# Performance work log

Measured on AMD Instinct MI355X. Metric: run time of the kernel, lower is better.

## Reference

```python
import jax, jax.numpy as jnp
import numpy as np

B, N, M = 2, 2048, 1024
C, CTX, H = 1024, 1024, 16
D = C // H
HID = int(C * 4.0)
EPS = 1e-6


def _ln(h):
    # LayerNorm32: fp32 layernorm, eps=1e-6, no affine params
    h32 = h.astype(jnp.float32)
    mu = jnp.mean(h32, axis=-1, keepdims=True)
    var = jnp.var(h32, axis=-1, keepdims=True)
    return ((h32 - mu) * jax.lax.rsqrt(var + EPS)).astype(h.dtype)


def _sdpa(q, k, v):
    # q: [B,Q,H,D], k/v: [B,K,H,D]
    scale = 1.0 / np.sqrt(D)
    s = jnp.einsum('bqhd,bkhd->bhqk', q, k) * scale
    p = jax.nn.softmax(s, axis=-1)
    return jnp.einsum('bhqk,bkhd->bqhd', p, v)


def _forward(x, context, Wqkv, bqkv, Wos, bos, Wq, bq, Wkv, bkv, Woc, boc, W1, b1, W2, b2):
    Bx, Nx, _ = x.shape
    Mx = context.shape[1]
    # --- self-attention (attn_mode='full') ---
    h = _ln(x)
    qkv = (h @ Wqkv + bqkv).reshape(Bx, Nx, 3, H, D)
    q, k, v = qkv[:, :, 0], qkv[:, :, 1], qkv[:, :, 2]
    a = _sdpa(q, k, v).reshape(Bx, Nx, C)
    x = x + (a @ Wos + bos)
    # --- cross-attention (always 'full') ---
    h = _ln(x)
    q = (h @ Wq + bq).reshape(Bx, Nx, H, D)
    kv = (context @ Wkv + bkv).reshape(Bx, Mx, 2, H, D)
    k, v = kv[:, :, 0], kv[:, :, 1]
    a = _sdpa(q, k, v).reshape(Bx, Nx, C)
    x = x + (a @ Woc + boc)
    # --- FFN with tanh-approx GELU ---
    h = _ln(x)
    x = x + (jax.nn.gelu(h @ W1 + b1, approximate=True) @ W2 + b2)
    return x


def setup_inputs() -> dict:
    key = jax.random.key(0)
    ks = jax.random.split(key, 12)
    rn = lambda k, shape: (jax.random.normal(k, shape, jnp.float32) * 0.02)
    return {
        'x': jax.random.normal(ks[0], (B, N, C), jnp.float32),
        'context': jax.random.normal(ks[1], (B, M, CTX), jnp.float32),
        'Wqkv': rn(ks[2], (C, 3 * C)), 'bqkv': jnp.zeros((3 * C,), jnp.float32),
        'Wos': rn(ks[3], (C, C)), 'bos': jnp.zeros((C,), jnp.float32),
        'Wq': rn(ks[4], (C, C)), 'bq': jnp.zeros((C,), jnp.float32),
        'Wkv': rn(ks[5], (CTX, 2 * C)), 'bkv': jnp.zeros((2 * C,), jnp.float32),
        'Woc': rn(ks[6], (C, C)), 'boc': jnp.zeros((C,), jnp.float32),
        'W1': rn(ks[7], (C, HID)), 'b1': jnp.zeros((HID,), jnp.float32),
        'W2': rn(ks[8], (HID, C)), 'b2': jnp.zeros((C,), jnp.float32),
    }


def reference(x, context, Wqkv, bqkv, Wos, bos, Wq, bq, Wkv, bkv, Woc, boc, W1, b1, W2, b2):
    return _forward(x, context, Wqkv, bqkv, Wos, bos, Wq, bq, Wkv, bkv, Woc, boc, W1, b1, W2, b2)
```

## Files before the change

### kernel.cpp

```cpp
#include <hip/hip_runtime.h>
#include <cstdint>

typedef unsigned short u16;
typedef short bf16x8 __attribute__((ext_vector_type(8)));
typedef unsigned short u16x8 __attribute__((ext_vector_type(8)));
typedef float f32x4 __attribute__((ext_vector_type(4)));

__device__ __forceinline__ u16 f2bf(float f) {
  union { float f; uint32_t u; } v; v.f = f;
  uint32_t r = (v.u + 0x7fffu + ((v.u >> 16) & 1u)) >> 16;
  return (u16)r;
}

__device__ __forceinline__ void gload_lds16(const u16* g, u16* l) {
  __builtin_amdgcn_global_load_lds(
      (const __attribute__((address_space(1))) void*)g,
      (__attribute__((address_space(3))) void*)l, 16, 0, 0);
}

__global__ __launch_bounds__(256) void ln_kernel(const float* __restrict__ x,
                                                 u16* __restrict__ h) {
  const int row = blockIdx.x;
  const int tid = threadIdx.x;
  const float4 v = *reinterpret_cast<const float4*>(x + (long)row * 1024 + tid * 4);
  float s  = v.x + v.y + v.z + v.w;
  float ss = v.x * v.x + v.y * v.y + v.z * v.z + v.w * v.w;
#pragma unroll
  for (int off = 32; off >= 1; off >>= 1) {
    s  += __shfl_xor(s, off, 64);
    ss += __shfl_xor(ss, off, 64);
  }
  __shared__ float red[8];
  const int wave = tid >> 6, lane = tid & 63;
  if (lane == 0) { red[wave] = s; red[4 + wave] = ss; }
  __syncthreads();
  s  = red[0] + red[1] + red[2] + red[3];
  ss = red[4] + red[5] + red[6] + red[7];
  const float mu   = s * (1.0f / 1024.0f);
  const float var  = ss * (1.0f / 1024.0f) - mu * mu;
  const float rstd = rsqrtf(var + 1e-6f);
  ushort4 o;
  o.x = f2bf((v.x - mu) * rstd);
  o.y = f2bf((v.y - mu) * rstd);
  o.z = f2bf((v.z - mu) * rstd);
  o.w = f2bf((v.w - mu) * rstd);
  *reinterpret_cast<ushort4*>(h + (long)row * 1024 + tid * 4) = o;
}

struct WEnt { const float* W; u16* Wt; int K, N, tEnd; };
struct WEnts { WEnt e[7]; int n; };

__global__ __launch_bounds__(256) void wconvert_all(WEnts args) {
  __shared__ u16 tile[64][72];
  int t = blockIdx.x;
  int i = 0, tStart = 0;
  while (i < args.n - 1 && t >= args.e[i].tEnd) { tStart = args.e[i].tEnd; i++; }
  const float* W = args.e[i].W;
  u16* Wt = args.e[i].Wt;
  const int K = args.e[i].K, N = args.e[i].N;
  const int rel = t - tStart;
  const int ntn = N >> 6;
  const int tn = rel % ntn, tk = rel / ntn;
  const int n0 = tn * 64, k0 = tk * 64;

  const int th = threadIdx.x;
  const int c4 = (th & 15) * 4;
  const int r  = th >> 4;
#pragma unroll
  for (int ii = 0; ii < 4; ii++) {
    const int row = ii * 16 + r;
    const float4 v = *reinterpret_cast<const float4*>(W + (long)(k0 + row) * N + n0 + c4);
    tile[c4 + 0][row] = f2bf(v.x);
    tile[c4 + 1][row] = f2bf(v.y);
    tile[c4 + 2][row] = f2bf(v.z);
    tile[c4 + 3][row] = f2bf(v.w);
  }
  __syncthreads();
  const int c8 = (th & 7) * 8;
  const int rn = th >> 3;
#pragma unroll
  for (int ii = 0; ii < 2; ii++) {
    const int row = ii * 32 + rn;
    *reinterpret_cast<u16x8*>(Wt + (long)(n0 + row) * K + k0 + c8) =
        *reinterpret_cast<const u16x8*>(&tile[row][c8]);
  }
}

__global__ __launch_bounds__(256) void f2bf_kernel(const float* __restrict__ in,
                                                   u16* __restrict__ out) {
  const long i = ((long)blockIdx.x * 256 + threadIdx.x) * 4;
  const float4 v = *reinterpret_cast<const float4*>(in + i);
  ushort4 o;
  o.x = f2bf(v.x); o.y = f2bf(v.y); o.z = f2bf(v.z); o.w = f2bf(v.w);
  *reinterpret_cast<ushort4*>(out + i) = o;
}

__global__ __launch_bounds__(256) void vtrans(const u16* __restrict__ V,
                                              u16* __restrict__ Vt,
                                              int vStride, long vBatch, int nk) {
  __shared__ u16 tile[64][72];
  const int t = threadIdx.x;
  const int b = blockIdx.z, h = blockIdx.y, n0 = blockIdx.x * 64;
  const u16* vp = V + (long)b * vBatch + h * 64;
  u16* op = Vt + (long)(b * 16 + h) * 64 * (long)nk + n0;
  const int ch = t & 7;
#pragma unroll
  for (int i = 0; i < 2; i++) {
    const int n = (t >> 3) + i * 32;
    const u16x8 v = *reinterpret_cast<const u16x8*>(vp + (long)(n0 + n) * vStride + ch * 8);
#pragma unroll
    for (int j = 0; j < 8; j++) tile[ch * 8 + j][n] = v[j];
  }
  __syncthreads();
#pragma unroll
  for (int i = 0; i < 2; i++) {
    const int d = (t >> 3) + i * 32;
    *reinterpret_cast<u16x8*>(op + (long)d * nk + ch * 8) =
        *reinterpret_cast<const u16x8*>(&tile[d][ch * 8]);
  }
}

template <int TN, bool OUT_BF16, bool GELU_ACT, bool RES, int KSPLIT>
__device__ __forceinline__ void gemm_core(
    const u16* __restrict__ A, const u16* __restrict__ Bt,
    const float* __restrict__ bias, const float* __restrict__ res,
    void* __restrict__ Cout, int Ndim, int Kdim, int m0, int n0,
    u16* Al, u16* Bl) {
  constexpr int NFRAG = TN / 32;
  const int tid  = threadIdx.x;
  const int lane = tid & 63, wave = tid >> 6;
  const int quad = lane >> 4, l15 = lane & 15;
  const int wr = wave >> 1, wc = wave & 1;

  f32x4 acc[4][NFRAG];
  const f32x4 vzero = {0.f, 0.f, 0.f, 0.f};
#pragma unroll
  for (int i = 0; i < 4; i++)
#pragma unroll
    for (int jj = 0; jj < NFRAG; jj++) acc[i][jj] = vzero;

  const int Keff = Kdim / KSPLIT;
  const long kOff = (KSPLIT > 1) ? (long)blockIdx.y * Keff : 0;

  const long rowOff = (long)(lane >> 2) * Kdim + (((lane & 3) ^ ((lane >> 3) & 3)) * 8);
  const u16* gA = A  + (long)m0 * Kdim + rowOff + kOff;
  const u16* gB = Bt + (long)n0 * Kdim + rowOff + kOff;

  auto stage = [&](int k0, int p) {
    gload_lds16(gA + (long)(wave * 16) * Kdim + k0,       Al + p * 4096 + wave * 512);
    gload_lds16(gA + (long)((wave + 4) * 16) * Kdim + k0, Al + p * 4096 + (wave + 4) * 512);
    gload_lds16(gB + (long)(wave * 16) * Kdim + k0,       Bl + p * (TN * 32) + wave * 512);
    if constexpr (TN == 128)
      gload_lds16(gB + (long)((wave + 4) * 16) * Kdim + k0, Bl + p * (TN * 32) + (wave + 4) * 512);
  };

  const int swz = (quad ^ ((l15 >> 1) & 3)) * 8;

  stage(0, 0);
  int p = 0;
  for (int k0 = 0; k0 < Keff; k0 += 32, p ^= 1) {
    __syncthreads();
    bf16x8 af[4], bfr[NFRAG];
#pragma unroll
    for (int mt = 0; mt < 4; mt++)
      af[mt] = *reinterpret_cast<const bf16x8*>(Al + p * 4096 + (wr * 64 + mt * 16 + l15) * 32 + swz);
#pragma unroll
    for (int nt = 0; nt < NFRAG; nt++)
      bfr[nt] = *reinterpret_cast<const bf16x8*>(Bl + p * (TN * 32) + (wc * NFRAG * 16 + nt * 16 + l15) * 32 + swz);
    if (k0 + 32 < Keff) stage(k0 + 32, p ^ 1);
#pragma unroll
    for (int mt = 0; mt < 4; mt++)
#pragma unroll
      for (int nt = 0; nt < NFRAG; nt++)
        acc[mt][nt] = __builtin_amdgcn_mfma_f32_16x16x32_bf16(af[mt], bfr[nt], acc[mt][nt], 0, 0, 0);
  }

#pragma unroll
  for (int nt = 0; nt < NFRAG; nt++) {
    const int col = n0 + wc * NFRAG * 16 + nt * 16 + l15;
    const float bv = bias[col];
#pragma unroll
    for (int mt = 0; mt < 4; mt++) {
#pragma unroll
      for (int r = 0; r < 4; r++) {
        const int row = m0 + wr * 64 + mt * 16 + quad * 4 + r;
        if constexpr (KSPLIT > 1) {
          float y = acc[mt][nt][r];
          if (blockIdx.y == 0) y += bv;
          unsafeAtomicAdd(&((float*)Cout)[(long)row * Ndim + col], y);
        } else {
          float y = acc[mt][nt][r] + bv;
          if (GELU_ACT) {
            const float t = 0.7978845608028654f * (y + 0.044715f * y * y * y);
            y = 0.5f * y * (1.0f + tanhf(t));
          }
          if (RES) y += res[(long)row * Ndim + col];
          if (OUT_BF16)
            ((u16*)Cout)[(long)row * Ndim + col] = f2bf(y);
          else
            ((float*)Cout)[(long)row * Ndim + col] = y;
        }
      }
    }
  }
}

template <int TN, int SX, bool OUT_BF16, bool GELU_ACT, bool RES, int KSPLIT = 1>
__global__ __launch_bounds__(256, 2) void gemm_bt(
    const u16* __restrict__ A, const u16* __restrict__ Bt,
    const float* __restrict__ bias, const float* __restrict__ res,
    void* __restrict__ Cout, int Ndim, int Kdim, int lx, int ly) {
  __shared__ u16 Al[2 * 128 * 32];
  __shared__ u16 Bl[2 * TN * 32];
  const int j = blockIdx.x;
  const int c = j & 7, kk = j >> 3;
  const int cx = c % SX, cy = c / SX;
  const int bx = cx * lx + (kk % lx);
  const int by = cy * ly + (kk / lx);
  gemm_core<TN, OUT_BF16, GELU_ACT, RES, KSPLIT>(
      A, Bt, bias, res, Cout, Ndim, Kdim, by * 128, bx * TN, Al, Bl);
}

struct GemmSeg {
  const u16* A; const u16* Bt; const float* bias; u16* C;
  int Ndim, Kdim, SX, lx, ly;
};
struct GemmDualP { GemmSeg s0, s1; int nBlk0; };

template <int TN>
__global__ __launch_bounds__(256, 2) void gemm_dual(GemmDualP pp) {
  __shared__ u16 Al[2 * 128 * 32];
  __shared__ u16 Bl[2 * TN * 32];
  int j = blockIdx.x;
  GemmSeg s;
  if (j < pp.nBlk0) { s = pp.s0; } else { s = pp.s1; j -= pp.nBlk0; }
  const int c = j & 7, kk = j >> 3;
  const int cx = c % s.SX, cy = c / s.SX;
  const int bx = cx * s.lx + (kk % s.lx);
  const int by = cy * s.ly + (kk / s.lx);
  gemm_core<TN, true, false, false, 1>(
      s.A, s.Bt, s.bias, nullptr, s.C, s.Ndim, s.Kdim, by * 128, bx * TN, Al, Bl);
}

__global__ __launch_bounds__(256, 2) void attn_kernel(
    const u16* __restrict__ Q, const u16* __restrict__ K, const u16* __restrict__ Vt,
    u16* __restrict__ O, int nk, int qStride, int kStride, int oStride,
    long qBatch, long kBatch, long oBatch) {
  __shared__ u16 Kt[2][64 * 64];
  __shared__ u16 Vl[2][64 * 64];
  __shared__ u16 Pl[4][32 * 64];

  const int tid = threadIdx.x;
  const int lane = tid & 63, wave = tid >> 6;
  const int quad = lane >> 4, l15 = lane & 15;
  const int b = blockIdx.z, hh = blockIdx.y, qt = blockIdx.x;

  const u16* qp = Q + (long)b * qBatch + hh * 64;
  const u16* kp = K + (long)b * kBatch + hh * 64;
  const u16* vp = Vt + (long)(b * 16 + hh) * 64 * (long)nk;

  bf16x8 qf[2][2];
  const int qrow = qt * 128 + wave * 32 + l15;
#pragma unroll
  for (int qg = 0; qg < 2; qg++) {
    qf[qg][0] = *reinterpret_cast<const bf16x8*>(qp + (long)(qrow + qg * 16) * qStride + quad * 8);
    qf[qg][1] = *reinterpret_cast<const bf16x8*>(qp + (long)(qrow + qg * 16) * qStride + 32 + quad * 8);
  }

  const int r8 = lane >> 3;
  const int gcol = ((lane & 7) ^ r8) * 8;
  const u16* kgA = kp + (long)(wave * 8 + r8) * kStride + gcol;
  const u16* kgB = kp + (long)((wave + 4) * 8 + r8) * kStride + gcol;
  const u16* vgA = vp + (long)(wave * 8 + r8) * nk + gcol;
  const u16* vgB = vp + (long)((wave + 4) * 8 + r8) * nk + gcol;

  const int cF = (quad ^ (l15 & 7)) * 8;

  const f32x4 vzero = {0.f, 0.f, 0.f, 0.f};
  f32x4 oAcc[2][4];
  float lSt[2] = {0.f, 0.f};
#pragma unroll
  for (int qg = 0; qg < 2; qg++)
#pragma unroll
    for (int i = 0; i < 4; i++) oAcc[qg][i] = vzero;

  const float SCL = 0.18033688f;
  const int nTiles = nk >> 6;
  const long kAdv = (long)64 * kStride;

  auto stage = [&](int kt, int p) {
    gload_lds16(kgA + kt * kAdv, &Kt[p][wave * 512]);
    gload_lds16(kgB + kt * kAdv, &Kt[p][(wave + 4) * 512]);
    gload_lds16(vgA + kt * 64,   &Vl[p][wave * 512]);
    gload_lds16(vgB + kt * 64,   &Vl[p][(wave + 4) * 512]);
  };

  stage(0, 0);
  int p = 0;
  for (int kt = 0; kt < nTiles; kt++, p ^= 1) {
    __syncthreads();
    if (kt + 1 < nTiles) stage(kt + 1, p ^ 1);

    f32x4 st[2][4];
#pragma unroll
    for (int mt = 0; mt < 4; mt++) {
      const bf16x8 kf0 = *reinterpret_cast<const bf16x8*>(&Kt[p][(mt * 16 + l15) * 64 + cF]);
      const bf16x8 kf1 = *reinterpret_cast<const bf16x8*>(&Kt[p][(mt * 16 + l15) * 64 + (cF ^ 32)]);
#pragma unroll
      for (int qg = 0; qg < 2; qg++) {
        f32x4 z = vzero;
        z = __builtin_amdgcn_mfma_f32_16x16x32_bf16(kf0, qf[qg][0], z, 0, 0, 0);
        z = __builtin_amdgcn_mfma_f32_16x16x32_bf16(kf1, qf[qg][1], z, 0, 0, 0);
        st[qg][mt] = z;
      }
    }

#pragma unroll
    for (int qg = 0; qg < 2; qg++) {
      float ps = 0.f;
#pragma unroll
      for (int mt = 0; mt < 4; mt++)
#pragma unroll
        for (int r = 0; r < 4; r++) {
          const float pw = __builtin_amdgcn_exp2f(st[qg][mt][r] * SCL);
          st[qg][mt][r] = pw;
          ps += pw;
        }
      lSt[qg] += ps;
      u16* plw = &Pl[wave][(qg * 16 + l15) * 64];
#pragma unroll
      for (int mt = 0; mt < 4; mt++) {
        union { float f; uint32_t u; } a0, a1, a2, a3;
        a0.f = st[qg][mt][0]; a1.f = st[qg][mt][1];
        a2.f = st[qg][mt][2]; a3.f = st[qg][mt][3];
        a0.u += 0x8000u; a1.u += 0x8000u; a2.u += 0x8000u; a3.u += 0x8000u;
        uint2 w;
        w.x = __builtin_amdgcn_perm(a1.u, a0.u, 0x07060302u);
        w.y = __builtin_amdgcn_perm(a3.u, a2.u, 0x07060302u);
        const int pcol = (((mt * 2 + (quad >> 1)) ^ (l15 & 7)) * 8) + (quad & 1) * 4;
        *reinterpret_cast<uint2*>(&plw[pcol]) = w;
      }
    }

    bf16x8 pf[2][2];
#pragma unroll
    for (int qg = 0; qg < 2; qg++) {
      const u16* plw = &Pl[wave][(qg * 16 + l15) * 64];
      pf[qg][0] = *reinterpret_cast<const bf16x8*>(&plw[cF]);
      pf[qg][1] = *reinterpret_cast<const bf16x8*>(&plw[cF ^ 32]);
    }
#pragma unroll
    for (int dt = 0; dt < 4; dt++) {
      const bf16x8 vf0 = *reinterpret_cast<const bf16x8*>(&Vl[p][(dt * 16 + l15) * 64 + cF]);
      const bf16x8 vf1 = *reinterpret_cast<const bf16x8*>(&Vl[p][(dt * 16 + l15) * 64 + (cF ^ 32)]);
#pragma unroll
      for (int qg = 0; qg < 2; qg++) {
        oAcc[qg][dt] = __builtin_amdgcn_mfma_f32_16x16x32_bf16(pf[qg][0], vf0, oAcc[qg][dt], 0, 0, 0);
        oAcc[qg][dt] = __builtin_amdgcn_mfma_f32_16x16x32_bf16(pf[qg][1], vf1, oAcc[qg][dt], 0, 0, 0);
      }
    }
  }

  u16* op = O + (long)b * oBatch + hh * 64;
#pragma unroll
  for (int qg = 0; qg < 2; qg++) {
    float l = lSt[qg];
    l += __shfl_xor(l, 16, 64);
    l += __shfl_xor(l, 32, 64);
    float lR[4];
#pragma unroll
    for (int r = 0; r < 4; r++) lR[r] = 1.0f / __shfl(l, quad * 4 + r, 64);
#pragma unroll
    for (int dt = 0; dt < 4; dt++)
#pragma unroll
      for (int r = 0; r < 4; r++) {
        const int row = qt * 128 + wave * 32 + qg * 16 + quad * 4 + r;
        op[(long)row * oStride + dt * 16 + l15] = f2bf(oAcc[qg][dt][r] * lR[r]);
      }
  }
}

extern "C" void kernel_launch(void* const* d_in, const int* in_sizes, int n_in,
                              void* d_out, int out_size, void* d_ws, size_t ws_size,
                              hipStream_t stream) {
  const float* x    = (const float*)d_in[0];
  const float* ctx  = (const float*)d_in[1];
  const float* Wqkv = (const float*)d_in[2];
  const float* bqkv = (const float*)d_in[3];
  const float* Wos  = (const float*)d_in[4];
  const float* bos  = (const float*)d_in[5];
  const float* Wq   = (const float*)d_in[6];
  const float* bq   = (const float*)d_in[7];
  const float* Wkv  = (const float*)d_in[8];
  const float* bkv  = (const float*)d_in[9];
  const float* Woc  = (const float*)d_in[10];
  const float* boc  = (const float*)d_in[11];
  const float* W1   = (const float*)d_in[12];
  const float* b1   = (const float*)d_in[13];
  const float* W2   = (const float*)d_in[14];
  const float* b2   = (const float*)d_in[15];
  float* out = (float*)d_out;
  char* ws = (char*)d_ws;
  const size_t MB = 1024 * 1024;

  u16* h      = (u16*)ws;
  u16* abuf   = (u16*)(ws + 8 * MB);
  u16* wbuf   = (u16*)(ws + 8 * MB);
  u16* qkv    = (u16*)(ws + 16 * MB);
  u16* Wqkvt  = (u16*)(ws + 40 * MB);
  u16* Wost   = (u16*)(ws + 16 * MB);
  u16* Wqt    = (u16*)(ws + 18 * MB);
  u16* Wkvt   = (u16*)(ws + 20 * MB);
  u16* Woct   = (u16*)(ws + 24 * MB);
  u16* q2     = (u16*)(ws + 26 * MB);
  u16* kv2    = (u16*)(ws + 34 * MB);
  u16* ctxbf  = (u16*)(ws + 42 * MB);
  u16* VtCr   = (u16*)(ws + 16 * MB);
  u16* hid    = (u16*)(ws + 16 * MB);
  u16* VtSelf = h;
  u16* W1t    = wbuf;
  u16* W2t    = wbuf;

  WEnts w1; w1.n = 1;

  ln_kernel<<<dim3(4096), dim3(256), 0, stream>>>(x, h);
  w1.e[0] = {Wqkv, Wqkvt, 1024, 3072, 768};
  wconvert_all<<<dim3(768), dim3(256), 0, stream>>>(w1);
  gemm_bt<128, 2, true, false, false><<<dim3(768), dim3(256), 0, stream>>>(
      h, Wqkvt, bqkv, nullptr, qkv, 3072, 1024, 12, 8);
  vtrans<<<dim3(32, 16, 2), dim3(256), 0, stream>>>(
      qkv + 2048, VtSelf, 3072, (long)2048 * 3072, 2048);
  attn_kernel<<<dim3(16, 16, 2), dim3(256), 0, stream>>>(
      qkv, qkv + 1024, VtSelf, abuf, 2048, 3072, 3072, 1024,
      (long)2048 * 3072, (long)2048 * 3072, (long)2048 * 1024);

  WEnts w4; w4.n = 4;
  w4.e[0] = {Wos, Wost, 1024, 1024, 256};
  w4.e[1] = {Wq,  Wqt,  1024, 1024, 512};
  w4.e[2] = {Wkv, Wkvt, 1024, 2048, 1024};
  w4.e[3] = {Woc, Woct, 1024, 1024, 1280};
  wconvert_all<<<dim3(1280), dim3(256), 0, stream>>>(w4);
  f2bf_kernel<<<dim3(2048), dim3(256), 0, stream>>>(ctx, ctxbf);

  gemm_bt<64, 1, false, false, true><<<dim3(512), dim3(256), 0, stream>>>(
      abuf, Wost, bos, x, out, 1024, 1024, 16, 4);
  ln_kernel<<<dim3(4096), dim3(256), 0, stream>>>(out, h);

  GemmDualP dp;
  dp.s0 = {h,     Wqt,  bq,  q2,  1024, 1024, 1, 16, 4};
  dp.s1 = {ctxbf, Wkvt, bkv, kv2, 2048, 1024, 2, 16, 4};
  dp.nBlk0 = 512;
  gemm_dual<64><<<dim3(1024), dim3(256), 0, stream>>>(dp);
  vtrans<<<dim3(16, 16, 2), dim3(256), 0, stream>>>(
      kv2 + 1024, VtCr, 2048, (long)1024 * 2048, 1024);
  attn_kernel<<<dim3(16, 16, 2), dim3(256), 0, stream>>>(
      q2, kv2, VtCr, abuf, 1024, 1024, 2048, 1024,
      (long)2048 * 1024, (long)1024 * 2048, (long)2048 * 1024);
  gemm_bt<64, 1, false, false, false, 2><<<dim3(512, 2), dim3(256), 0, stream>>>(
      abuf, Woct, boc, nullptr, out, 1024, 1024, 16, 4);

  ln_kernel<<<dim3(4096), dim3(256), 0, stream>>>(out, h);
  w1.e[0] = {W1, W1t, 1024, 4096, 1024};
  wconvert_all<<<dim3(1024), dim3(256), 0, stream>>>(w1);
  gemm_bt<128, 2, true, true, false><<<dim3(1024), dim3(256), 0, stream>>>(
      h, W1t, b1, nullptr, hid, 4096, 1024, 16, 8);
  w1.e[0] = {W2, W2t, 4096, 1024, 1024};
  wconvert_all<<<dim3(1024), dim3(256), 0, stream>>>(w1);
  gemm_bt<128, 2, false, false, false, 4><<<dim3(256, 4), dim3(256), 0, stream>>>(
      hid, W2t, b2, nullptr, out, 1024, 4096, 4, 8);
}
```

Measured before the change: 520.9 us.

## Triple-buffer GEMM LDS pipeline with vmcnt waits and adjust split-K choices

After: 492.8 us. -5.4%, faster.

```diff
diff --git a/kernel.cpp b/kernel.cpp
--- a/kernel.cpp
+++ b/kernel.cpp
@@ -147,32 +147,53 @@
   const u16* gB = Bt + (long)n0 * Kdim + rowOff + kOff;
 
   auto stage = [&](int k0, int p) {
-    gload_lds16(gA + (long)(wave * 16) * Kdim + k0,       Al + p * 4096 + wave * 512);
-    gload_lds16(gA + (long)((wave + 4) * 16) * Kdim + k0, Al + p * 4096 + (wave + 4) * 512);
-    gload_lds16(gB + (long)(wave * 16) * Kdim + k0,       Bl + p * (TN * 32) + wave * 512);
+    u16* ab = Al + p * 4096;
+    u16* bb = Bl + p * (TN * 32);
+    gload_lds16(gA + (long)(wave * 16) * Kdim + k0,       ab + wave * 512);
+    gload_lds16(gA + (long)((wave + 4) * 16) * Kdim + k0, ab + (wave + 4) * 512);
+    gload_lds16(gB + (long)(wave * 16) * Kdim + k0,       bb + wave * 512);
     if constexpr (TN == 128)
-      gload_lds16(gB + (long)((wave + 4) * 16) * Kdim + k0, Bl + p * (TN * 32) + (wave + 4) * 512);
+      gload_lds16(gB + (long)((wave + 4) * 16) * Kdim + k0, bb + (wave + 4) * 512);
   };
 
   const int swz = (quad ^ ((l15 >> 1) & 3)) * 8;
 
   stage(0, 0);
-  int p = 0;
-  for (int k0 = 0; k0 < Keff; k0 += 32, p ^= 1) {
-    __syncthreads();
+  stage(32, 1);
+  int bufC = 0;
+  for (int k0 = 0; k0 < Keff; k0 += 32) {
+    if (k0 + 32 < Keff) {
+      if constexpr (TN == 128) asm volatile("s_waitcnt vmcnt(4)" ::: "memory");
+      else                     asm volatile("s_waitcnt vmcnt(3)" ::: "memory");
+    } else {
+      asm volatile("s_waitcnt vmcnt(0)" ::: "memory");
+    }
+    __builtin_amdgcn_s_barrier();
+
     bf16x8 af[4], bfr[NFRAG];
+    const u16* ab = Al + bufC * 4096;
+    const u16* bb = Bl + bufC * (TN * 32);
 #pragma unroll
     for (int mt = 0; mt < 4; mt++)
-      af[mt] = *reinterpret_cast<const bf16x8*>(Al + p * 4096 + (wr * 64 + mt * 16 + l15) * 32 + swz);
+      af[mt] = *reinterpret_cast<const bf16x8*>(ab + (wr * 64 + mt * 16 + l15) * 32 + swz);
 #pragma unroll
     for (int nt = 0; nt < NFRAG; nt++)
-      bfr[nt] = *reinterpret_cast<const bf16x8*>(Bl + p * (TN * 32) + (wc * NFRAG * 16 + nt * 16 + l15) * 32 + swz);
-    if (k0 + 32 < Keff) stage(k0 + 32, p ^ 1);
+      bfr[nt] = *reinterpret_cast<const bf16x8*>(bb + (wc * NFRAG * 16 + nt * 16 + l15) * 32 + swz);
+
+    if (k0 + 64 < Keff) {
+      int bn = bufC + 2; if (bn >= 3) bn -= 3;
+      stage(k0 + 64, bn);
+    }
+
+    __builtin_amdgcn_s_setprio(1);
 #pragma unroll
     for (int mt = 0; mt < 4; mt++)
 #pragma unroll
       for (int nt = 0; nt < NFRAG; nt++)
         acc[mt][nt] = __builtin_amdgcn_mfma_f32_16x16x32_bf16(af[mt], bfr[nt], acc[mt][nt], 0, 0, 0);
+    __builtin_amdgcn_s_setprio(0);
+
+    bufC = (bufC == 2) ? 0 : bufC + 1;
   }
 
 #pragma unroll
@@ -210,8 +231,8 @@
     const u16* __restrict__ A, const u16* __restrict__ Bt,
     const float* __restrict__ bias, const float* __restrict__ res,
     void* __restrict__ Cout, int Ndim, int Kdim, int lx, int ly) {
-  __shared__ u16 Al[2 * 128 * 32];
-  __shared__ u16 Bl[2 * TN * 32];
+  __shared__ u16 Al[3 * 128 * 32];
+  __shared__ u16 Bl[3 * TN * 32];
   const int j = blockIdx.x;
   const int c = j & 7, kk = j >> 3;
   const int cx = c % SX, cy = c / SX;
@@ -229,8 +250,8 @@
 
 template <int TN>
 __global__ __launch_bounds__(256, 2) void gemm_dual(GemmDualP pp) {
-  __shared__ u16 Al[2 * 128 * 32];
-  __shared__ u16 Bl[2 * TN * 32];
+  __shared__ u16 Al[3 * 128 * 32];
+  __shared__ u16 Bl[3 * TN * 32];
   int j = blockIdx.x;
   GemmSeg s;
   if (j < pp.nBlk0) { s = pp.s0; } else { s = pp.s1; j -= pp.nBlk0; }
@@ -456,8 +477,8 @@
   attn_kernel<<<dim3(16, 16, 2), dim3(256), 0, stream>>>(
       q2, kv2, VtCr, abuf, 1024, 1024, 2048, 1024,
       (long)2048 * 1024, (long)1024 * 2048, (long)2048 * 1024);
-  gemm_bt<64, 1, false, false, false, 2><<<dim3(512, 2), dim3(256), 0, stream>>>(
-      abuf, Woct, boc, nullptr, out, 1024, 1024, 16, 4);
+  gemm_bt<64, 1, false, false, true><<<dim3(512), dim3(256), 0, stream>>>(
+      abuf, Woct, boc, out, out, 1024, 1024, 16, 4);
 
   ln_kernel<<<dim3(4096), dim3(256), 0, stream>>>(out, h);
   w1.e[0] = {W1, W1t, 1024, 4096, 1024};
@@ -466,6 +487,6 @@
       h, W1t, b1, nullptr, hid, 4096, 1024, 16, 8);
   w1.e[0] = {W2, W2t, 4096, 1024, 1024};
   wconvert_all<<<dim3(1024), dim3(256), 0, stream>>>(w1);
-  gemm_bt<128, 2, false, false, false, 4><<<dim3(256, 4), dim3(256), 0, stream>>>(
+  gemm_bt<128, 2, false, false, false, 2><<<dim3(256, 2), dim3(256), 0, stream>>>(
       hid, W2t, b2, nullptr, out, 1024, 4096, 4, 8);
 }
```
